# Kernel tuning notes

Measured on AMD Instinct MI355X. Metric: run time of the kernel, lower is better.

The kernel has to match this reference:

```python
import jax, jax.numpy as jnp
from jax import lax
import numpy as np

# ---- dims / neuron params (match init_kwargs) ----
B, T, ENC, HID = 256, 500, 700, 128
TAU_MEM = 20.0      # tauSr == tauRef == tau_mem
THETA = 1.0         # spike_threshold
SCALE_REF = 1.0
WIDTH_GRAD = 1.0    # tauRho (surrogate width)
SCALE_GRAD = 1.0    # scaleRho (surrogate scale)


def alpha_filter(x, tau, mult):
    """Causal convolution along axis 0 with SLAYER's alpha (SRM) kernel
    h[k] = mult * (k/tau) * exp(1 - k/tau), Ts = 1.  Implemented as an exact
    2-state linear recurrence instead of an O(T^2) FIR conv.
    x: (T, ...) -> y: (T, ...)
    """
    d = jnp.exp(-1.0 / tau)          # per-step decay
    c = mult * jnp.exp(1.0) / tau    # h[k] = c * k * d**k

    def step(carry, xt):
        p, q = carry
        qn = d * q + c * d * p       # output at t (h[0] = 0)
        pn = d * p + xt
        return (pn, qn), qn

    z = jnp.zeros_like(x[0])
    _, y = lax.scan(step, (z, z), x)
    return y


def _spike_core(u):
    """SLAYER getSpikes: at each t, membrane = psp + accumulated refractory
    response (alpha kernel with mult = -2*theta*scaleRef, tau = tauRef) of all
    past spikes; emit spike (1/Ts) when membrane >= theta.
    u: (T, B, C) psp values -> (spikes, post-refractory membrane), both (T, B, C).
    """
    d = jnp.exp(-1.0 / TAU_MEM)
    c = (-2.0 * THETA * SCALE_REF) * jnp.exp(1.0) / TAU_MEM

    def step(carry, ut):
        p, q = carry
        qn = d * q + c * d * p       # refractory contribution at t (0 from spike at t)
        u_t = ut + qn                # membrane after refractory subtraction
        s_t = (u_t >= THETA).astype(ut.dtype)
        pn = d * p + s_t
        return (pn, qn), (s_t, u_t)

    z = jnp.zeros_like(u[0])
    _, (s, u_post) = lax.scan(step, (z, z), u)
    return s, u_post


@jax.custom_vjp
def spike(u):
    return _spike_core(u)[0]


def _spike_fwd(u):
    s, u_post = _spike_core(u)
    return s, u_post


def _spike_bwd(u_post, g):
    # SLAYER surrogate: pdf = scaleRho / (tauRho*theta) * exp(-|u - theta| / (tauRho*theta)),
    # evaluated on the refractory-modified membrane; grad does not flow through
    # the refractory recurrence (matches the torch autograd.Function).
    tc = WIDTH_GRAD * THETA
    pdf = (SCALE_GRAD / tc) * jnp.exp(-jnp.abs(u_post - THETA) / tc)
    return (g * pdf,)


spike.defvjp(_spike_fwd, _spike_bwd)


def setup_inputs():
    key = jax.random.key(0)
    k1, k2, k3 = jax.random.split(key, 3)
    # sparse binary input spike trains (B, T, ENC)
    x = (jax.random.uniform(k1, (B, T, ENC)) < 0.05).astype(jnp.float32)
    w1 = jax.random.normal(k2, (HID, ENC), dtype=jnp.float32) * 0.1
    w2 = jax.random.normal(k3, (1, HID), dtype=jnp.float32) * 0.3
    return {"x": x, "w1": w1, "w2": w2}


def reference(x, w1, w2):
    # x: (B, T, ENC) -> time-major (T, B, ENC) for the temporal scans
    xt = jnp.transpose(x, (1, 0, 2))
    h = jnp.einsum('tbc,hc->tbh', xt, w1)        # slayer.dense (bias-free linear per step)
    h = alpha_filter(h, TAU_MEM, 1.0)            # slayer.psp
    s1 = spike(h)                                # slayer.spike (threshold + refractory)
    o = jnp.einsum('tbh,oh->tbo', s1, w2)
    o = alpha_filter(o, TAU_MEM, 1.0)
    s2 = spike(o)
    return jnp.transpose(s2, (1, 0, 2))          # (B, T, 1), matches out2.movedim(-1, 1)
```

## Files before the change

kernel.cpp:

```cpp
#include <hip/hip_runtime.h>

#define BB  256
#define TT  500
#define ENC 700
#define ENC_PAD 704
#define HID 128

__global__ __launch_bounds__(128) void transpose_w1_kernel(const float* __restrict__ w1,
                                                           float* __restrict__ w1t) {
    int c = blockIdx.x;
    int h = threadIdx.x;
    w1t[c * HID + h] = (c < ENC) ? w1[h * ENC + c] : 0.0f;
}

__global__ __launch_bounds__(256, 4) void spmm4_kernel(const float* __restrict__ x,
                                                       const float* __restrict__ w1t,
                                                       float* __restrict__ h) {
    __shared__ ushort lists[8][152];
    const int lane = threadIdx.x & 63;
    const int w = threadIdx.x >> 6;
    const int rbase = blockIdx.x * 8 + w * 2;
    const unsigned long long lt = (1ull << lane) - 1ull;

    const float* xrowA = x + (size_t)rbase * ENC;
    const float* xrowB = xrowA + ENC;
    float xva[11], xvb[11];
    #pragma unroll
    for (int k = 0; k < 11; ++k) {
        int c = k * 64 + lane;
        xva[k] = (c < ENC) ? xrowA[c] : 0.0f;
    }
    #pragma unroll
    for (int k = 0; k < 11; ++k) {
        int c = k * 64 + lane;
        xvb[k] = (c < ENC) ? xrowB[c] : 0.0f;
    }

    int nA = 0, nB = 0;
    #pragma unroll
    for (int k = 0; k < 11; ++k) {
        bool act = (xva[k] != 0.0f);
        unsigned long long m = __ballot(act);
        if (act) {
            int pos = nA + (int)__popcll(m & lt);
            if (pos < 144) lists[2 * w + 0][pos] = (ushort)(k * 64 + lane);
        }
        nA += (int)__popcll(m);
    }
    #pragma unroll
    for (int k = 0; k < 11; ++k) {
        bool act = (xvb[k] != 0.0f);
        unsigned long long m = __ballot(act);
        if (act) {
            int pos = nB + (int)__popcll(m & lt);
            if (pos < 144) lists[2 * w + 1][pos] = (ushort)(k * 64 + lane);
        }
        nB += (int)__popcll(m);
    }
    nA = (nA < 144) ? nA : 144;
    nB = (nB < 144) ? nB : 144;
    int npmax = ((nA > nB ? nA : nB) + 3) & ~3;
    if (npmax < 4) npmax = 4;
    for (int p = nA + lane; p < npmax + 4; p += 64) lists[2 * w + 0][p] = (ushort)ENC;
    for (int p = nB + lane; p < npmax + 4; p += 64) lists[2 * w + 1][p] = (ushort)ENC;

    const int half = lane >> 5;
    const int hl = lane & 31;
    const ushort* mylist = lists[2 * w + half];
    const float* wb = w1t + 4 * hl;

    float a0 = 0.f, a1 = 0.f, a2 = 0.f, a3 = 0.f;

    int c0 = mylist[0], c1 = mylist[1], c2 = mylist[2], c3 = mylist[3];
    float4 p0 = *(const float4*)(wb + (size_t)c0 * HID);
    float4 p1 = *(const float4*)(wb + (size_t)c1 * HID);
    float4 p2 = *(const float4*)(wb + (size_t)c2 * HID);
    float4 p3 = *(const float4*)(wb + (size_t)c3 * HID);

    for (int j = 0; j < npmax; j += 4) {
        int d0 = mylist[j + 4], d1 = mylist[j + 5];
        int d2 = mylist[j + 6], d3 = mylist[j + 7];
        float4 q0 = *(const float4*)(wb + (size_t)d0 * HID);
        float4 q1 = *(const float4*)(wb + (size_t)d1 * HID);
        float4 q2 = *(const float4*)(wb + (size_t)d2 * HID);
        float4 q3 = *(const float4*)(wb + (size_t)d3 * HID);
        a0 += p0.x; a1 += p0.y; a2 += p0.z; a3 += p0.w;
        a0 += p1.x; a1 += p1.y; a2 += p1.z; a3 += p1.w;
        a0 += p2.x; a1 += p2.y; a2 += p2.z; a3 += p2.w;
        a0 += p3.x; a1 += p3.y; a2 += p3.z; a3 += p3.w;
        p0 = q0; p1 = q1; p2 = q2; p3 = q3;
    }

    const int r = rbase + half;
    const int b = r / TT;
    const int t = r - b * TT;
    float4* dst = (float4*)(h + (size_t)t * (BB * HID) + (size_t)b * HID) + hl;
    *dst = make_float4(a0, a1, a2, a3);
}

__device__ __forceinline__ void async_copy4(const float* g, float* l) {
    __builtin_amdgcn_global_load_lds(
        (const __attribute__((address_space(1))) void*)g,
        (__attribute__((address_space(3))) void*)l,
        4, 0, 0);
}

__global__ __launch_bounds__(128) void recur_kernel(const float* __restrict__ hgl,
                                                    const float* __restrict__ w2,
                                                    float* __restrict__ out) {
    __shared__ float hbuf[2][50 * 128];
    __shared__ float vbuf[50 * 129];
    __shared__ float pbuf[2][50];

    const int b = blockIdx.x;
    const int tid = threadIdx.x;
    const int lane = tid & 63;
    const int w = tid >> 6;

    const float D   = 0.95122942450071400910f;
    const float CD  = (float)(0.13591409142295226 * 0.95122942450071400910);
    const float CRD = (float)(-0.27182818284590452 * 0.95122942450071400910);

    float ap = 0.f, aq = 0.f, rp = 0.f, rq = 0.f;
    float Ap = 0.f, Aq = 0.f, Rp = 0.f, Rq = 0.f;
    const float w2v = w2[tid];

    auto stage = [&](int chunk, int buf) {
        const int t0 = chunk * 50 + w * 25;
        #pragma unroll 5
        for (int i = 0; i < 25; ++i) {
            const float* g = hgl + (size_t)(t0 + i) * (BB * HID) + (size_t)b * HID + lane;
            float* l = &hbuf[buf][(w * 25 + i) * 128];
            async_copy4(g, l);
            async_copy4(g + 64, l + 64);
        }
    };

    stage(0, 0);
    __syncthreads();

    for (int chunk = 0; chunk < 10; ++chunk) {
        const int cur = chunk & 1;
        if (chunk < 9) stage(chunk + 1, cur ^ 1);

        const float* hb = &hbuf[cur][0];
        #pragma unroll
        for (int tl = 0; tl < 50; ++tl) {
            float hv = hb[tl * 128 + tid];
            float y = fmaf(D, aq, CD * ap);
            aq = y;
            ap = fmaf(D, ap, hv);
            float q = fmaf(D, rq, CRD * rp);
            float u = y + q;
            float s = (u >= 1.0f) ? 1.0f : 0.0f;
            rq = q;
            rp = fmaf(D, rp, s);
            vbuf[tl * 129 + tid] = s * w2v;
        }
        __syncthreads();

        if (tid < 50) {
            const float* row = &vbuf[tid * 129];
            float a0 = 0.f, a1 = 0.f, a2 = 0.f, a3 = 0.f;
            #pragma unroll
            for (int k = 0; k < 64; k += 4) {
                a0 += row[k]; a1 += row[k + 1]; a2 += row[k + 2]; a3 += row[k + 3];
            }
            pbuf[0][tid] = (a0 + a1) + (a2 + a3);
        } else if (tid >= 64 && tid < 114) {
            const float* row = &vbuf[(tid - 64) * 129 + 64];
            float a0 = 0.f, a1 = 0.f, a2 = 0.f, a3 = 0.f;
            #pragma unroll
            for (int k = 0; k < 64; k += 4) {
                a0 += row[k]; a1 += row[k + 1]; a2 += row[k + 2]; a3 += row[k + 3];
            }
            pbuf[1][tid - 64] = (a0 + a1) + (a2 + a3);
        }
        __syncthreads();

        float my_s2 = 0.f;
        #pragma unroll
        for (int tl = 0; tl < 50; ++tl) {
            float ot = pbuf[0][tl] + pbuf[1][tl];
            float y2 = fmaf(D, Aq, CD * Ap);
            Aq = y2;
            Ap = fmaf(D, Ap, ot);
            float q2 = fmaf(D, Rq, CRD * Rp);
            float u2 = y2 + q2;
            float s2 = (u2 >= 1.0f) ? 1.0f : 0.0f;
            Rq = q2;
            Rp = fmaf(D, Rp, s2);
            if (tl == tid) my_s2 = s2;
        }
        if (tid < 50) out[(size_t)b * TT + chunk * 50 + tid] = my_s2;
    }
}

extern "C" void kernel_launch(void* const* d_in, const int* in_sizes, int n_in,
                              void* d_out, int out_size, void* d_ws, size_t ws_size,
                              hipStream_t stream) {
    const float* x  = (const float*)d_in[0];
    const float* w1 = (const float*)d_in[1];
    const float* w2 = (const float*)d_in[2];
    float* out = (float*)d_out;

    float* h   = (float*)d_ws;
    float* w1t = h + (size_t)TT * BB * HID;

    hipLaunchKernelGGL(transpose_w1_kernel, dim3(ENC_PAD), dim3(HID), 0, stream, w1, w1t);
    hipLaunchKernelGGL(spmm4_kernel, dim3((BB * TT) / 8), dim3(256), 0, stream, x, w1t, h);
    hipLaunchKernelGGL(recur_kernel, dim3(BB), dim3(128), 0, stream, h, w2, out);
}
```

Baseline: 601.8 us.

## Store h batch-major and prefetch recurrence inputs into registers

The sparse matmul now writes h in (b,t) row order instead of time-major, so each recurrence block reads one contiguous slab. The recurrence kernel drops the LDS async-copy double buffer and loads each 50-step chunk straight into register arrays (hA/hB), ping-ponging so the next chunk's loads are in flight while the current one is computed. This removes LDS staging and barriers and gives better-localised global reads. The cost is about 100 extra live registers per thread, which may lower occupancy or cause spills.

```diff
diff --git a/kernel.cpp b/kernel.cpp
--- a/kernel.cpp
+++ b/kernel.cpp
@@ -92,30 +92,18 @@
     }
 
     const int r = rbase + half;
-    const int b = r / TT;
-    const int t = r - b * TT;
-    float4* dst = (float4*)(h + (size_t)t * (BB * HID) + (size_t)b * HID) + hl;
+    float4* dst = (float4*)(h + (size_t)r * HID) + hl;
     *dst = make_float4(a0, a1, a2, a3);
-}
-
-__device__ __forceinline__ void async_copy4(const float* g, float* l) {
-    __builtin_amdgcn_global_load_lds(
-        (const __attribute__((address_space(1))) void*)g,
-        (__attribute__((address_space(3))) void*)l,
-        4, 0, 0);
 }
 
 __global__ __launch_bounds__(128) void recur_kernel(const float* __restrict__ hgl,
                                                     const float* __restrict__ w2,
                                                     float* __restrict__ out) {
-    __shared__ float hbuf[2][50 * 128];
     __shared__ float vbuf[50 * 129];
     __shared__ float pbuf[2][50];
 
     const int b = blockIdx.x;
     const int tid = threadIdx.x;
-    const int lane = tid & 63;
-    const int w = tid >> 6;
 
     const float D   = 0.95122942450071400910f;
     const float CD  = (float)(0.13591409142295226 * 0.95122942450071400910);
@@ -125,31 +113,17 @@
     float Ap = 0.f, Aq = 0.f, Rp = 0.f, Rq = 0.f;
     const float w2v = w2[tid];
 
-    auto stage = [&](int chunk, int buf) {
-        const int t0 = chunk * 50 + w * 25;
-        #pragma unroll 5
-        for (int i = 0; i < 25; ++i) {
-            const float* g = hgl + (size_t)(t0 + i) * (BB * HID) + (size_t)b * HID + lane;
-            float* l = &hbuf[buf][(w * 25 + i) * 128];
-            async_copy4(g, l);
-            async_copy4(g + 64, l + 64);
-        }
-    };
-
-    stage(0, 0);
-    __syncthreads();
-
-    for (int chunk = 0; chunk < 10; ++chunk) {
-        const int cur = chunk & 1;
-        if (chunk < 9) stage(chunk + 1, cur ^ 1);
-
-        const float* hb = &hbuf[cur][0];
+    const float* hb = hgl + (size_t)b * (TT * HID) + tid;
+
+    float hA[50], hB[50];
+
+    auto body = [&](const float (&hv)[50], int chunk) {
         #pragma unroll
         for (int tl = 0; tl < 50; ++tl) {
-            float hv = hb[tl * 128 + tid];
+            float h_ = hv[tl];
             float y = fmaf(D, aq, CD * ap);
             aq = y;
-            ap = fmaf(D, ap, hv);
+            ap = fmaf(D, ap, h_);
             float q = fmaf(D, rq, CRD * rp);
             float u = y + q;
             float s = (u >= 1.0f) ? 1.0f : 0.0f;
@@ -193,6 +167,24 @@
             if (tl == tid) my_s2 = s2;
         }
         if (tid < 50) out[(size_t)b * TT + chunk * 50 + tid] = my_s2;
+    };
+
+    #pragma unroll
+    for (int j = 0; j < 50; ++j) hA[j] = hb[j * HID];
+
+    for (int cp = 0; cp < 5; ++cp) {
+        {
+            const float* g = hb + (size_t)(2 * cp + 1) * 50 * HID;
+            #pragma unroll
+            for (int j = 0; j < 50; ++j) hB[j] = g[j * HID];
+        }
+        body(hA, 2 * cp);
+        if (cp < 4) {
+            const float* g = hb + (size_t)(2 * cp + 2) * 50 * HID;
+            #pragma unroll
+            for (int j = 0; j < 50; ++j) hA[j] = g[j * HID];
+        }
+        body(hB, 2 * cp + 1);
     }
 }
 
```

After: 590.4 us. No clear change (-1.9%).
